# Performance work log

Hardware: AMD Instinct MI355X
Metric: run time of the kernel (lower is better)

Reference implementation:

```python
import jax, jax.numpy as jnp
import numpy as np

CHANNELS = 2
IMG_H = 32
IMG_DIM = IMG_H * IMG_H * CHANNELS      # 2048
IMG_QUBITS = 11
ALL_QUBITS = 12
COM_DIM = 128
COM_QUBITS = 7
LAYERS = 4
BATCH = 4096
HIDDEN = 512


def setup_inputs() -> dict:
    key = jax.random.key(0)
    k = jax.random.split(key, 5)
    x = jax.random.normal(k[0], (BATCH, CHANNELS, IMG_H, IMG_H), dtype=jnp.float32)
    W1 = jax.random.normal(k[1], (IMG_DIM, HIDDEN), dtype=jnp.float32) * (1.0 / np.sqrt(IMG_DIM))
    b1 = jnp.zeros((HIDDEN,), jnp.float32)
    W2 = jax.random.normal(k[2], (HIDDEN, COM_DIM), dtype=jnp.float32) * (1.0 / np.sqrt(HIDDEN))
    b2 = jnp.zeros((COM_DIM,), jnp.float32)
    asz_params = jax.random.uniform(k[3], (LAYERS, ALL_QUBITS, 3), jnp.float32, 0.0, np.pi)
    return {"x": x, "W1": W1, "b1": b1, "W2": W2, "b2": b2, "asz_params": asz_params}


def _apply_1q(state, mat, wire):
    # state: (B,) + (2,)*ALL_QUBITS ; apply 2x2 complex mat on `wire` (axis wire+1)
    s = jnp.moveaxis(state, wire + 1, -1)
    s = jnp.einsum('ij,...j->...i', mat, s)
    return jnp.moveaxis(s, -1, wire + 1)


def _cnot(state, ctrl, tgt):
    s = jnp.moveaxis(state, (ctrl + 1, tgt + 1), (-2, -1))
    s = jnp.concatenate([s[..., 0:1, :], s[..., 1:2, ::-1]], axis=-2)
    return jnp.moveaxis(s, (-2, -1), (ctrl + 1, tgt + 1))


def _frqi(state, params, q):
    # Uniformly-controlled RY on wire 0; controls = wires 1..q.
    # PennyLane loop: index's bit j (LSB=bit0, via reversed binary string) is the
    # control value on wire j+1 -> bit-reversed relative to C-order axis flattening.
    B = state.shape[0]
    rest = 2 ** (ALL_QUBITS - 1 - q)
    ang = params.reshape((B,) + (2,) * q)
    ang = jnp.transpose(ang, (0,) + tuple(range(q, 0, -1))).reshape(B, 2 ** q)
    c = jnp.cos(ang * 0.5)[:, :, None]
    sn = jnp.sin(ang * 0.5)[:, :, None]
    s = state.reshape(B, 2, 2 ** q, rest)
    s0, s1 = s[:, 0], s[:, 1]
    new = jnp.stack([c * s0 - sn * s1, sn * s0 + c * s1], axis=1)
    return new.reshape((B,) + (2,) * ALL_QUBITS)


def _rot_matrix(phi, theta, omega):
    # PennyLane Rot = RZ(omega) RY(theta) RZ(phi)
    c, s = jnp.cos(theta * 0.5), jnp.sin(theta * 0.5)
    m00 = jnp.exp(-0.5j * (phi + omega)) * c
    m01 = -jnp.exp(0.5j * (phi - omega)) * s
    m10 = jnp.exp(-0.5j * (phi - omega)) * s
    m11 = jnp.exp(0.5j * (phi + omega)) * c
    return jnp.stack([jnp.stack([m00, m01]), jnp.stack([m10, m11])]).astype(jnp.complex64)


def _circuit(com_params, img_params, asz_params):
    B = com_params.shape[0]
    state = jnp.zeros((B, 2 ** ALL_QUBITS), jnp.complex64).at[:, 0].set(1.0)
    state = state.reshape((B,) + (2,) * ALL_QUBITS)
    H = (jnp.array([[1.0, 1.0], [1.0, -1.0]]) / np.sqrt(2.0)).astype(jnp.complex64)
    for w in range(1, COM_QUBITS + 1):
        state = _apply_1q(state, H, w)
    state = _frqi(state, com_params, COM_QUBITS)
    # StronglyEntanglingLayers: per layer, Rot on every wire then CNOT ring of range r
    n = ALL_QUBITS
    for l in range(LAYERS):
        for w in range(n):
            state = _apply_1q(state, _rot_matrix(asz_params[l, w, 0], asz_params[l, w, 1], asz_params[l, w, 2]), w)
        r = (l % (n - 1)) + 1
        for w in range(n):
            state = _cnot(state, w, (w + r) % n)
    state = _frqi(state, img_params, IMG_QUBITS)
    for w in range(1, IMG_QUBITS + 1):
        state = _apply_1q(state, H, w)
    # expval of H = -1 * PauliZ(0)  ->  P(wire0=1) - P(wire0=0)
    s = state.reshape(B, 2, -1)
    probs = jnp.sum(s.real ** 2 + s.imag ** 2, axis=-1)
    return probs[:, 1] - probs[:, 0]


def reference(x, W1, b1, W2, b2, asz_params):
    B = x.shape[0]
    xf = x.reshape(B, -1)
    com_params = jnp.maximum(xf @ W1 + b1, 0.0) @ W2 + b2   # classical compression net
    img_params = -xf                                        # x = -1 * x in torch forward
    return _circuit(com_params, img_params, asz_params)
```

## Files before the change

kernel.cpp:

```cpp
#include <hip/hip_runtime.h>
#include <stdint.h>
#include <math.h>


typedef __attribute__((ext_vector_type(4))) float f32x4;
typedef __attribute__((ext_vector_type(2))) float f32x2;
typedef __attribute__((ext_vector_type(8))) short bf16x8;
typedef __attribute__((ext_vector_type(8))) unsigned short u16x8;
typedef __attribute__((ext_vector_type(4))) unsigned short u16x4;

struct QArgs {
  uint16_t xcs[12][16];
  uint16_t anp[12][8];
  uint8_t  gm8[12][4];
  uint32_t cmb_t[8];
  uint32_t cmb_q[8];
  uint32_t smF8;
};
static_assert(sizeof(QArgs) <= 1024, "kernarg too big");

__device__ __host__ __forceinline__ int swz(int j) { return j ^ (j >> 5) ^ (j >> 10); }

__device__ __forceinline__ unsigned short f2bf(float x) {
  unsigned u = __float_as_uint(x);
  unsigned r = (u + 0x7fffu + ((u >> 16) & 1u)) >> 16;
  return (unsigned short)r;
}
__device__ __forceinline__ float bf2f(unsigned short h) {
  return __uint_as_float(((unsigned)h) << 16);
}
__device__ __forceinline__ float xsign(float v, unsigned sgn) {
  return __uint_as_float(__float_as_uint(v) ^ sgn);
}

__device__ __forceinline__ f32x2 pkmul(f32x2 a, f32x2 b) {
  f32x2 d;
  asm("v_pk_mul_f32 %0, %1, %2" : "=v"(d) : "v"(a), "v"(b));
  return d;
}
__device__ __forceinline__ f32x2 pkfma(f32x2 a, f32x2 b, f32x2 c) {
  f32x2 d = c;
  asm("v_pk_fma_f32 %0, %1, %2, %0" : "+v"(d) : "v"(a), "v"(b));
  return d;
}
__device__ __forceinline__ f32x2 pkfma_swapneglo(f32x2 a, f32x2 b, f32x2 c) {
  f32x2 d = c;
  asm("v_pk_fma_f32 %0, %1, %2, %0 op_sel:[0,1,0] op_sel_hi:[1,0,1] neg_lo:[0,1,0]"
      : "+v"(d) : "v"(a), "v"(b));
  return d;
}
__device__ __forceinline__ f32x2 pkfma_swapneghi(f32x2 a, f32x2 b, f32x2 c) {
  f32x2 d = c;
  asm("v_pk_fma_f32 %0, %1, %2, %0 op_sel:[0,1,0] op_sel_hi:[1,0,1] neg_hi:[0,1,0]"
      : "+v"(d) : "v"(a), "v"(b));
  return d;
}
__device__ __forceinline__ f32x2 pkfma_negboth(f32x2 a, f32x2 b, f32x2 c) {
  f32x2 d = c;
  asm("v_pk_fma_f32 %0, %1, %2, %0 neg_lo:[0,1,0] neg_hi:[0,1,0]"
      : "+v"(d) : "v"(a), "v"(b));
  return d;
}

__device__ __forceinline__ void bfly(f32x2& A, f32x2& B,
                                     f32x2 G0, f32x2 S1, f32x2 S2, f32x2 G3) {
  f32x2 na = pkmul(G0, A);
  na = pkfma_swapneglo(S1, A, na);
  na = pkfma(S2, B, na);
  na = pkfma_swapneglo(G3, B, na);
  f32x2 nb = pkmul(G0, B);
  nb = pkfma_swapneghi(S1, B, nb);
  nb = pkfma_negboth(S2, A, nb);
  nb = pkfma_swapneglo(G3, A, nb);
  A = na;
  B = nb;
}

__global__ __launch_bounds__(256) void conv_x_kernel(const float* __restrict__ x,
                                                     unsigned short* __restrict__ A3) {
  int g = blockIdx.x * 256 + threadIdx.x;
  int m = g >> 8;
  int c8 = (g & 255) << 3;
  const float4* src = (const float4*)(x + (size_t)m * 2048 + c8);
  float4 v0 = src[0], v1 = src[1];
  float vs[8] = {v0.x, v0.y, v0.z, v0.w, v1.x, v1.y, v1.z, v1.w};
  u16x8 h8, l8;
#pragma unroll
  for (int i = 0; i < 8; ++i) {
    unsigned short h = f2bf(vs[i]);
    h8[i] = h;
    l8[i] = f2bf(vs[i] - bf2f(h));
  }
  size_t base = (size_t)m * 6144 + c8;
  *(u16x8*)(A3 + base)        = h8;
  *(u16x8*)(A3 + base + 2048) = h8;
  *(u16x8*)(A3 + base + 4096) = l8;
}

__global__ __launch_bounds__(256) void conv_w_kernel(const float* __restrict__ W,
                                                     unsigned short* __restrict__ BT,
                                                     int K, int N) {
  __shared__ float tile[64][65];
  int k0 = blockIdx.x * 64, n0 = blockIdx.y * 64;
  int t = threadIdx.x;
  int li = t >> 2;
  int lj = (t & 3) << 4;
  const float* src = W + (size_t)(k0 + li) * N + n0 + lj;
#pragma unroll
  for (int c = 0; c < 16; c += 4) {
    float4 v = *(const float4*)(src + c);
    tile[li][lj + c + 0] = v.x; tile[li][lj + c + 1] = v.y;
    tile[li][lj + c + 2] = v.z; tile[li][lj + c + 3] = v.w;
  }
  __syncthreads();
  int n = n0 + li;
  int kk = lj;
  u16x8 hi2[2], lo2[2];
#pragma unroll
  for (int c = 0; c < 16; ++c) {
    float v = tile[kk + c][li];
    unsigned short h = f2bf(v);
    hi2[c >> 3][c & 7] = h;
    lo2[c >> 3][c & 7] = f2bf(v - bf2f(h));
  }
  size_t rb = (size_t)n * (3 * (size_t)K) + k0 + kk;
  *(u16x8*)(BT + rb)         = hi2[0];
  *(u16x8*)(BT + rb + 8)     = hi2[1];
  *(u16x8*)(BT + rb + K)     = lo2[0];
  *(u16x8*)(BT + rb + K + 8) = lo2[1];
  *(u16x8*)(BT + rb + 2*K)     = hi2[0];
  *(u16x8*)(BT + rb + 2*K + 8) = hi2[1];
}

__global__ __launch_bounds__(256) void gemm_part(
    const unsigned short* __restrict__ A, const unsigned short* __restrict__ B,
    float* __restrict__ P, int M, int N, int K, int KS) {
  constexpr int BK = 64;
  __shared__ unsigned short smA[64 * BK];
  __shared__ unsigned short smB[64 * BK];
  const int t = threadIdx.x, wave = t >> 6, lane = t & 63;
  const int m0 = blockIdx.x * 64, n0 = blockIdx.y * 64;
  const int k0 = blockIdx.z * KS, k1 = k0 + KS;
  const int wr = wave >> 1, wc = wave & 1;

  f32x4 acc00 = (f32x4)0.f, acc01 = (f32x4)0.f;
  f32x4 acc10 = (f32x4)0.f, acc11 = (f32x4)0.f;

  const int off0 = t * 16, off1 = (256 + t) * 16;
  const int ar0 = off0 >> 7, ac0 = off0 & 127;
  const int ar1 = off1 >> 7, ac1 = off1 & 127;
  const int ad0 = off0 ^ ((ar0 & 7) << 4);
  const int ad1 = off1 ^ ((ar1 & 7) << 4);
  const char* Ab0 = (const char*)A + ((size_t)(m0 + ar0) * K) * 2 + ac0;
  const char* Ab1 = (const char*)A + ((size_t)(m0 + ar1) * K) * 2 + ac1;
  const char* Bb0 = (const char*)B + ((size_t)(n0 + ar0) * K) * 2 + ac0;
  const char* Bb1 = (const char*)B + ((size_t)(n0 + ar1) * K) * 2 + ac1;

  const int la = lane & 15;
  const int kb0 = (lane >> 4) * 16;
  const int rA0 = wr * 32 + la,      rA1 = wr * 32 + 16 + la;
  const int rB0 = wc * 32 + la,      rB1 = wc * 32 + 16 + la;
  const int oA0 = (rA0 * 128 + kb0) ^ ((rA0 & 7) << 4);
  const int oA1 = (rA1 * 128 + kb0) ^ ((rA1 & 7) << 4);
  const int oB0 = (rB0 * 128 + kb0) ^ ((rB0 & 7) << 4);
  const int oB1 = (rB1 * 128 + kb0) ^ ((rB1 & 7) << 4);

  uint4 ra0 = *(const uint4*)(Ab0 + (size_t)k0 * 2);
  uint4 ra1 = *(const uint4*)(Ab1 + (size_t)k0 * 2);
  uint4 rb0 = *(const uint4*)(Bb0 + (size_t)k0 * 2);
  uint4 rb1 = *(const uint4*)(Bb1 + (size_t)k0 * 2);

  for (int kt = k0; kt < k1; kt += BK) {
    __syncthreads();
    *(uint4*)((char*)smA + ad0) = ra0;
    *(uint4*)((char*)smA + ad1) = ra1;
    *(uint4*)((char*)smB + ad0) = rb0;
    *(uint4*)((char*)smB + ad1) = rb1;
    __syncthreads();
    const int ktn = kt + BK;
    if (ktn < k1) {
      ra0 = *(const uint4*)(Ab0 + (size_t)ktn * 2);
      ra1 = *(const uint4*)(Ab1 + (size_t)ktn * 2);
      rb0 = *(const uint4*)(Bb0 + (size_t)ktn * 2);
      rb1 = *(const uint4*)(Bb1 + (size_t)ktn * 2);
    }
#pragma unroll
    for (int kk = 0; kk < 2; ++kk) {
      const int kb = kk * 64;
      bf16x8 af0 = *(const bf16x8*)((const char*)smA + (oA0 ^ kb));
      bf16x8 af1 = *(const bf16x8*)((const char*)smA + (oA1 ^ kb));
      bf16x8 bf0 = *(const bf16x8*)((const char*)smB + (oB0 ^ kb));
      bf16x8 bf1 = *(const bf16x8*)((const char*)smB + (oB1 ^ kb));
      acc00 = __builtin_amdgcn_mfma_f32_16x16x32_bf16(af0, bf0, acc00, 0, 0, 0);
      acc01 = __builtin_amdgcn_mfma_f32_16x16x32_bf16(af0, bf1, acc01, 0, 0, 0);
      acc10 = __builtin_amdgcn_mfma_f32_16x16x32_bf16(af1, bf0, acc10, 0, 0, 0);
      acc11 = __builtin_amdgcn_mfma_f32_16x16x32_bf16(af1, bf1, acc11, 0, 0, 0);
    }
  }

  float* Pz = P + (size_t)blockIdx.z * M * N;
  const int r0 = (lane >> 4) * 4;
  const int cn = lane & 15;
  const int mA = m0 + wr * 32 + r0;
  const int nA = n0 + wc * 32 + cn;
#pragma unroll
  for (int r = 0; r < 4; ++r) {
    Pz[(size_t)(mA + r) * N + nA]           = acc00[r];
    Pz[(size_t)(mA + r) * N + nA + 16]      = acc01[r];
    Pz[(size_t)(mA + 16 + r) * N + nA]      = acc10[r];
    Pz[(size_t)(mA + 16 + r) * N + nA + 16] = acc11[r];
  }
}

__global__ __launch_bounds__(256) void reduce_h3_kernel(
    const float* __restrict__ P, const float* __restrict__ bias,
    unsigned short* __restrict__ Hb) {
  const int M = 4096, N = 512;
  int g = blockIdx.x * 256 + threadIdx.x;
  int m = g >> 7;
  int n4 = (g & 127) << 2;
  const float* p = P + (size_t)m * N + n4;
  float4 v0 = *(const float4*)p;
  float4 v1 = *(const float4*)(p + (size_t)M * N);
  float4 vb = *(const float4*)(bias + n4);
  float r[4] = {v0.x + v1.x + vb.x, v0.y + v1.y + vb.y,
                v0.z + v1.z + vb.z, v0.w + v1.w + vb.w};
  u16x4 h4, l4;
#pragma unroll
  for (int i = 0; i < 4; ++i) {
    float v = fmaxf(r[i], 0.0f);
    unsigned short h = f2bf(v);
    h4[i] = h;
    l4[i] = f2bf(v - bf2f(h));
  }
  size_t rbase = (size_t)m * 1536;
  *(u16x4*)(Hb + rbase + n4)        = h4;
  *(u16x4*)(Hb + rbase + 512 + n4)  = h4;
  *(u16x4*)(Hb + rbase + 1024 + n4) = l4;
}

__global__ __launch_bounds__(256) void reduce_com_kernel(
    const float* __restrict__ P, const float* __restrict__ bias,
    float* __restrict__ com) {
  const int M = 4096, N = 128;
  int g = blockIdx.x * 256 + threadIdx.x;
  int m = g >> 5;
  int n4 = (g & 31) << 2;
  const float* p = P + (size_t)m * N + n4;
  const size_t slab = (size_t)M * N;
  float4 a0 = *(const float4*)p;
  float4 a1 = *(const float4*)(p + slab);
  float4 a2 = *(const float4*)(p + 2 * slab);
  float4 a3 = *(const float4*)(p + 3 * slab);
  float4 vb = *(const float4*)(bias + n4);
  float4 r;
  r.x = a0.x + a1.x + a2.x + a3.x + vb.x;
  r.y = a0.y + a1.y + a2.y + a3.y + vb.y;
  r.z = a0.z + a1.z + a2.z + a3.z + vb.z;
  r.w = a0.w + a1.w + a2.w + a3.w + vb.w;
  *(float4*)(com + (size_t)m * N + n4) = r;
}

__global__ __launch_bounds__(64) void prep_gates(const float* __restrict__ asz,
                                                 float* __restrict__ gcoef) {
  int t = threadIdx.x;
  if (t < 48) {
    float phi = asz[t * 3 + 0], th = asz[t * 3 + 1], om = asz[t * 3 + 2];
    float sth, cth, sa, ca, sb, cb;
    sincosf(0.5f * th, &sth, &cth);
    sincosf(0.5f * (phi + om), &sa, &ca);
    sincosf(0.5f * (phi - om), &sb, &cb);
    float4 g;
    g.x =  ca * cth;
    g.y = -sa * cth;
    g.z = -cb * sth;
    g.w = -sb * sth;
    ((float4*)gcoef)[t] = g;
  }
}

__global__ __launch_bounds__(256) void quantum_kernel(
    const float* __restrict__ x, const float* __restrict__ com,
    const float* __restrict__ gcoef, float* __restrict__ out, QArgs qa) {
  __shared__ f32x2 st[4096];
  __shared__ float xrow[2048];
  const int t = threadIdx.x;
  const int b = blockIdx.x;
  const float4* __restrict__ gc4 = (const float4*)gcoef;

  {
    const float4* xs = (const float4*)(x + (size_t)b * 2048);
    ((float4*)xrow)[t] = xs[t];
    ((float4*)xrow)[t + 256] = xs[t + 256];
  }
#pragma unroll
  for (int s = 0; s < 16; ++s) st[s * 256 + t] = (f32x2){0.f, 0.f};
  __syncthreads();

  {
    int jj = t & 127, b0 = t >> 7;
    int p = __brev((unsigned)jj) >> 25;
    float ang = 0.5f * com[(size_t)b * 128 + p];
    float s = __sinf(ang), c = __cosf(ang);
    float val = (b0 ? s : c) * 0.08838834764831845f;
    int j = (b0 << 11) | (jj << 4);
    *(f32x2*)((char*)st + (swz(j) << 3)) = (f32x2){val, 0.f};
  }
  __syncthreads();

#pragma unroll 1
  for (int p = 0; p < 12; ++p) {
    int srB = 0;
#pragma unroll
    for (int i = 0; i < 8; ++i) srB ^= ((t >> i) & 1) ? (int)qa.anp[p][i] : 0;

    const int gi = (p / 3) * 12 + (p % 3) * 4;
    float4 gk0 = gc4[gi + 0], gk1 = gc4[gi + 1], gk2 = gc4[gi + 2], gk3 = gc4[gi + 3];
    unsigned sg0 = (unsigned)__popc(t & (int)qa.gm8[p][0]) << 31;
    unsigned sg1 = (unsigned)__popc(t & (int)qa.gm8[p][1]) << 31;
    unsigned sg2 = (unsigned)__popc(t & (int)qa.gm8[p][2]) << 31;
    unsigned sg3 = (unsigned)__popc(t & (int)qa.gm8[p][3]) << 31;

    int aB[16];
    f32x2 v[16];
#pragma unroll
    for (int s = 0; s < 16; ++s) {
      aB[s] = srB ^ (int)qa.xcs[p][s];
      v[s] = *(const f32x2*)((const char*)st + aB[s]);
    }

#pragma unroll
    for (int k = 0; k < 4; ++k) {
      float4 g = (k == 0) ? gk0 : (k == 1) ? gk1 : (k == 2) ? gk2 : gk3;
      unsigned sg = (k == 0) ? sg0 : (k == 1) ? sg1 : (k == 2) ? sg2 : sg3;
      f32x2 G0 = (f32x2)(g.x);
      f32x2 S1 = (f32x2)(xsign(g.y, sg));
      f32x2 S2 = (f32x2)(xsign(g.z, sg));
      f32x2 G3 = (f32x2)(g.w);
      const int bk = 1 << k;
#pragma unroll
      for (int s = 0; s < 16; ++s) {
        if (s & bk) continue;
        bfly(v[s], v[s | bk], G0, S1, S2, G3);
      }
    }
#pragma unroll
    for (int s = 0; s < 16; ++s) *(f32x2*)((char*)st + aB[s]) = v[s];
    __syncthreads();
  }

  float accv = 0.f;
  {
    unsigned C0 = 0;
#pragma unroll
    for (int i = 0; i < 8; ++i) C0 ^= ((t >> i) & 1) ? qa.cmb_t[i] : 0u;
#pragma unroll
    for (int q = 0; q < 8; ++q) {
      unsigned C = C0 ^ qa.cmb_q[q];
      int aA = (int)(C & 0x7FF8u);
      int aB2 = aA ^ (int)qa.smF8;
      float ang = xrow[C >> 16];
      float sx = __sinf(ang), cx = __cosf(ang);
      f32x2 a = *(const f32x2*)((const char*)st + aA);
      f32x2 bb = *(const f32x2*)((const char*)st + aB2);
      float da = a.x * a.x + a.y * a.y;
      float db = bb.x * bb.x + bb.y * bb.y;
      float d = da - db;
      float dot = a.x * bb.x + a.y * bb.y;
      unsigned sgn = (C & 0x8000u) << 16;
      float dp = xsign(d, sgn);
      accv -= cx * dp + 2.0f * sx * dot;
    }
  }
  __syncthreads();

#pragma unroll
  for (int o = 32; o > 0; o >>= 1) accv += __shfl_down(accv, o, 64);
  if ((t & 63) == 0) xrow[t >> 6] = accv;
  __syncthreads();
  if (t == 0) out[b] = xrow[0] + xrow[1] + xrow[2] + xrow[3];
}

static inline int par16(int v) { return __builtin_popcount((unsigned)v) & 1; }

extern "C" void kernel_launch(void* const* d_in, const int* in_sizes, int n_in,
                              void* d_out, int out_size, void* d_ws, size_t ws_size,
                              hipStream_t stream) {
  (void)in_sizes; (void)n_in; (void)out_size; (void)ws_size;
  const float* x   = (const float*)d_in[0];
  const float* W1  = (const float*)d_in[1];
  const float* b1  = (const float*)d_in[2];
  const float* W2  = (const float*)d_in[3];
  const float* b2  = (const float*)d_in[4];
  const float* asz = (const float*)d_in[5];
  float* out = (float*)d_out;

  char* ws = (char*)d_ws;
  unsigned short* A3  = (unsigned short*)ws; ws += (size_t)4096 * 6144 * 2;
  unsigned short* B3T = (unsigned short*)ws; ws += (size_t)512 * 6144 * 2;
  unsigned short* H3  = (unsigned short*)ws; ws += (size_t)4096 * 1536 * 2;
  unsigned short* W23 = (unsigned short*)ws; ws += (size_t)128 * 1536 * 2;
  float* com = (float*)ws;                   ws += (size_t)4096 * 128 * 4;
  float* gcoef = (float*)ws;                 ws += (size_t)1024;
  float* P = (float*)ws;                     ws += (size_t)2 * 4096 * 512 * 4;

  QArgs qa;
  int cols[12], rows[12];
  for (int w = 0; w < 12; ++w) cols[w] = rows[w] = 1 << (11 - w);
  int hswz;
  for (int l = 0; l < 4; ++l) {
    for (int g = 0; g < 3; ++g) {
      int p = l * 3 + g;
      int m[4], grow[4];
      for (int k = 0; k < 4; ++k) {
        int w = g * 4 + k;
        m[k] = cols[w];
        grow[k] = rows[w];
      }
      for (int s = 0; s < 16; ++s) {
        int v = 0;
        for (int k = 0; k < 4; ++k)
          if (s & (1 << k)) v ^= m[k];
        hswz = v ^ (v >> 5) ^ (v >> 10);
        qa.xcs[p][s] = (uint16_t)(hswz << 3);
      }
      int mm[4] = {m[0], m[1], m[2], m[3]};
      int piv = 0;
      for (int k = 0; k < 4; ++k) {
        int pb = 31 - __builtin_clz((unsigned)mm[k]);
        piv |= 1 << pb;
        for (int k2 = k + 1; k2 < 4; ++k2)
          if (mm[k2] & (1 << pb)) mm[k2] ^= mm[k];
      }
      int npb[8], c = 0;
      for (int bit = 0; bit < 12; ++bit)
        if (!(piv & (1 << bit))) npb[c++] = bit;
      for (int i = 0; i < 8; ++i) {
        int bv = 1 << npb[i];
        hswz = bv ^ (bv >> 5) ^ (bv >> 10);
        qa.anp[p][i] = (uint16_t)(hswz << 3);
      }
      for (int k = 0; k < 4; ++k) {
        int mask8 = 0;
        for (int i = 0; i < 8; ++i)
          mask8 |= ((grow[k] >> npb[i]) & 1) << i;
        qa.gm8[p][k] = (uint8_t)mask8;
      }
    }
    int r = l % 11 + 1;
    for (int w = 0; w < 12; ++w) {
      int cw = w, tw = (w + r) % 12;
      cols[cw] ^= cols[tw];
      rows[tw] ^= rows[cw];
    }
  }
  {
    int mF = cols[0];
    int hb = 31 - __builtin_clz((unsigned)mF);
    int lowmask = (1 << hb) - 1;
    auto jAof = [&](int u) { return ((u & ~lowmask) << 1) | (u & lowmask); };
    auto cmbof = [&](int j) -> uint32_t {
      int pidx = 0;
      for (int w = 1; w < 12; ++w)
        pidx |= par16(j & rows[w]) << (w - 1);
      int rho = par16(j & rows[0]);
      int sj = j ^ (j >> 5) ^ (j >> 10);
      return ((uint32_t)pidx << 16) | ((uint32_t)rho << 15) | (uint32_t)(sj << 3);
    };
    for (int i = 0; i < 8; ++i) qa.cmb_t[i] = cmbof(jAof(1 << i));
    for (int q = 0; q < 8; ++q) qa.cmb_q[q] = cmbof(jAof(q << 8));
    int sF = mF ^ (mF >> 5) ^ (mF >> 10);
    qa.smF8 = (uint32_t)(sF << 3);
  }

  conv_x_kernel<<<4096, 256, 0, stream>>>(x, A3);
  conv_w_kernel<<<dim3(32, 8), 256, 0, stream>>>(W1, B3T, 2048, 512);
  conv_w_kernel<<<dim3(8, 2), 256, 0, stream>>>(W2, W23, 512, 128);
  prep_gates<<<1, 64, 0, stream>>>(asz, gcoef);
  gemm_part<<<dim3(64, 8, 2), 256, 0, stream>>>(A3, B3T, P, 4096, 512, 6144, 3072);
  reduce_h3_kernel<<<2048, 256, 0, stream>>>(P, b1, H3);
  gemm_part<<<dim3(64, 2, 4), 256, 0, stream>>>(H3, W23, P, 4096, 128, 1536, 384);
  reduce_com_kernel<<<512, 256, 0, stream>>>(P, b2, com);
  quantum_kernel<<<4096, 256, 0, stream>>>(x, com, gcoef, out, qa);
}
```

Before: 296.0 us.

## Use 128x128 MFMA GEMM tile with direct global-to-LDS loads for first layer

Adds a new GEMM kernel that computes a 128x128 output tile per block, with each wave doing a 4x4 grid of 16x16x32 bf16 MFMAs. Operands are loaded straight from global memory into LDS with global_load_lds and an XOR swizzle. The first layer's GEMM now uses this kernel with split-K 4 instead of 2, and the reduce kernel is widened to sum four partial slabs. The larger tile raises operand reuse and cuts the number of global loads per FLOP. In exchange it writes and reads twice as many fp32 partial sums, and the single-buffered K loop with no prefetch may stall on memory latency.

```diff
diff --git a/kernel.cpp b/kernel.cpp
--- a/kernel.cpp
+++ b/kernel.cpp
@@ -130,6 +130,90 @@
   *(u16x8*)(BT + rb + K + 8) = lo2[1];
   *(u16x8*)(BT + rb + 2*K)     = hi2[0];
   *(u16x8*)(BT + rb + 2*K + 8) = hi2[1];
+}
+
+__global__ __launch_bounds__(256) void gemm128(
+    const unsigned short* __restrict__ A, const unsigned short* __restrict__ B,
+    float* __restrict__ P, int M, int N, int K, int KS) {
+  constexpr int BK = 64;
+  __shared__ unsigned short smA[128 * BK];
+  __shared__ unsigned short smB[128 * BK];
+  const int t = threadIdx.x, wave = t >> 6, lane = t & 63;
+  const int m0 = blockIdx.x * 128, n0 = blockIdx.y * 128;
+  const int k0 = blockIdx.z * KS, k1 = k0 + KS;
+  const int wr = wave >> 1, wc = wave & 1;
+
+  f32x4 acc[4][4];
+#pragma unroll
+  for (int i = 0; i < 4; ++i)
+#pragma unroll
+    for (int j = 0; j < 4; ++j) acc[i][j] = (f32x4)0.0f;
+
+  const int rsub = t >> 3;
+  const int csw = ((t & 7) ^ (rsub & 7)) * 8;
+  const int ldsoff = wave * 1024;
+
+  const int q = lane >> 4, la = lane & 15;
+
+  for (int kt = k0; kt < k1; kt += BK) {
+#pragma unroll
+    for (int i = 0; i < 4; ++i) {
+      int row = i * 32 + rsub;
+      const unsigned short* ga = A + (size_t)(m0 + row) * K + kt + csw;
+      __builtin_amdgcn_global_load_lds(
+          (const __attribute__((address_space(1))) unsigned int*)ga,
+          (__attribute__((address_space(3))) unsigned int*)((char*)smA + i * 4096 + ldsoff),
+          16, 0, 0);
+    }
+#pragma unroll
+    for (int i = 0; i < 4; ++i) {
+      int row = i * 32 + rsub;
+      const unsigned short* gb = B + (size_t)(n0 + row) * K + kt + csw;
+      __builtin_amdgcn_global_load_lds(
+          (const __attribute__((address_space(1))) unsigned int*)gb,
+          (__attribute__((address_space(3))) unsigned int*)((char*)smB + i * 4096 + ldsoff),
+          16, 0, 0);
+    }
+    __syncthreads();
+
+#pragma unroll
+    for (int kk = 0; kk < 2; ++kk) {
+      bf16x8 af[4], bf[4];
+#pragma unroll
+      for (int mi = 0; mi < 4; ++mi) {
+        int row = wr * 64 + mi * 16 + la;
+        int off = row * 128 + (((q + 4 * kk) ^ (row & 7)) << 4);
+        af[mi] = *(const bf16x8*)((const char*)smA + off);
+      }
+#pragma unroll
+      for (int ni = 0; ni < 4; ++ni) {
+        int row = wc * 64 + ni * 16 + la;
+        int off = row * 128 + (((q + 4 * kk) ^ (row & 7)) << 4);
+        bf[ni] = *(const bf16x8*)((const char*)smB + off);
+      }
+#pragma unroll
+      for (int mi = 0; mi < 4; ++mi)
+#pragma unroll
+        for (int ni = 0; ni < 4; ++ni)
+          acc[mi][ni] = __builtin_amdgcn_mfma_f32_16x16x32_bf16(af[mi], bf[ni], acc[mi][ni], 0, 0, 0);
+    }
+    __syncthreads();
+  }
+
+  float* Pz = P + (size_t)blockIdx.z * M * N;
+  const int r0 = q * 4;
+#pragma unroll
+  for (int mi = 0; mi < 4; ++mi) {
+#pragma unroll
+    for (int ni = 0; ni < 4; ++ni) {
+      int n = n0 + wc * 64 + ni * 16 + la;
+#pragma unroll
+      for (int r = 0; r < 4; ++r) {
+        int m = m0 + wr * 64 + mi * 16 + r0 + r;
+        Pz[(size_t)m * N + n] = acc[mi][ni][r];
+      }
+    }
+  }
 }
 
 __global__ __launch_bounds__(256) void gemm_part(
@@ -220,11 +304,16 @@
   int m = g >> 7;
   int n4 = (g & 127) << 2;
   const float* p = P + (size_t)m * N + n4;
+  const size_t slab = (size_t)M * N;
   float4 v0 = *(const float4*)p;
-  float4 v1 = *(const float4*)(p + (size_t)M * N);
+  float4 v1 = *(const float4*)(p + slab);
+  float4 v2 = *(const float4*)(p + 2 * slab);
+  float4 v3 = *(const float4*)(p + 3 * slab);
   float4 vb = *(const float4*)(bias + n4);
-  float r[4] = {v0.x + v1.x + vb.x, v0.y + v1.y + vb.y,
-                v0.z + v1.z + vb.z, v0.w + v1.w + vb.w};
+  float r[4] = {v0.x + v1.x + v2.x + v3.x + vb.x,
+                v0.y + v1.y + v2.y + v3.y + vb.y,
+                v0.z + v1.z + v2.z + v3.z + vb.z,
+                v0.w + v1.w + v2.w + v3.w + vb.w};
   u16x4 h4, l4;
 #pragma unroll
   for (int i = 0; i < 4; ++i) {
@@ -402,7 +491,7 @@
   unsigned short* W23 = (unsigned short*)ws; ws += (size_t)128 * 1536 * 2;
   float* com = (float*)ws;                   ws += (size_t)4096 * 128 * 4;
   float* gcoef = (float*)ws;                 ws += (size_t)1024;
-  float* P = (float*)ws;                     ws += (size_t)2 * 4096 * 512 * 4;
+  float* P = (float*)ws;                     ws += (size_t)4 * 4096 * 512 * 4;
 
   QArgs qa;
   int cols[12], rows[12];
@@ -477,7 +566,7 @@
   conv_w_kernel<<<dim3(32, 8), 256, 0, stream>>>(W1, B3T, 2048, 512);
   conv_w_kernel<<<dim3(8, 2), 256, 0, stream>>>(W2, W23, 512, 128);
   prep_gates<<<1, 64, 0, stream>>>(asz, gcoef);
-  gemm_part<<<dim3(64, 8, 2), 256, 0, stream>>>(A3, B3T, P, 4096, 512, 6144, 3072);
+  gemm128<<<dim3(32, 4, 4), 256, 0, stream>>>(A3, B3T, P, 4096, 512, 6144, 1536);
   reduce_h3_kernel<<<2048, 256, 0, stream>>>(P, b1, H3);
   gemm_part<<<dim3(64, 2, 4), 256, 0, stream>>>(H3, W23, P, 4096, 128, 1536, 384);
   reduce_com_kernel<<<512, 256, 0, stream>>>(P, b2, com);
```

New measurement: 291.6 us. About the same (-1.5%).
